# Optimization experiments

Measured on AMD Instinct MI355X. Metric: run time of the kernel, lower is better.

## Reference

```python
import jax, jax.numpy as jnp
import numpy as np

B, N, F, H, F_ = 2048, 8192, 512, 8, 64

def setup_inputs() -> dict:
    key = jax.random.key(0)
    k1, k2, k3, k4 = jax.random.split(key, 4)
    X = jax.random.normal(k1, (B, F), dtype=jnp.float32)
    G = jax.random.normal(k2, (N, F), dtype=jnp.float32)
    W = jax.random.normal(k3, (H, F, F_), dtype=jnp.float32) * 0.05   # per-head kernels
    att = jax.random.normal(k4, (H, 2 * F_), dtype=jnp.float32) * 0.05  # per-head att kernels (2F_,1) flattened
    return {"X": X, "G": G, "W": W, "att": att}

def reference(X, G, W, att):
    f_ = W.shape[-1]
    # Per-head linear transforms
    WhX = jnp.einsum('bf,hfe->hbe', X, W)   # [H,B,F_]
    WhG = jnp.einsum('nf,hfe->hne', G, W)   # [H,N,F_]
    # concat([WhX_i, WhG_j]) @ a  ==  WhX_i @ a1 + WhG_j @ a2  -> avoids tiled [B*N,2F_]
    a1, a2 = att[:, :f_], att[:, f_:]
    e1 = jnp.einsum('hbe,he->hb', WhX, a1)  # [H,B]
    e2 = jnp.einsum('hne,he->hn', WhG, a2)  # [H,N]
    scores = e1[:, :, None] + e2[:, None, :]            # [H,B,N] pairwise logits
    attn = jax.nn.softmax(scores, axis=-1)              # softmax over graph nodes
    out = jnp.einsum('hbn,hne->hbe', attn, WhG)         # weighted aggregate [H,B,F_]
    out = jax.nn.relu(out)                              # concat-mode applies activation per head
    # concat heads -> [B, H*F_]
    return jnp.transpose(out, (1, 0, 2)).reshape(out.shape[1], -1)
```

## Files before the change

### kernel.cpp

```cpp
#include <hip/hip_runtime.h>


#define HF   8
#define FDIM 512
#define FE   64
#define NG   8192
#define BX   2048
#define K2B  256
#define ROWS (NG / K2B)

#define WS_W2 16
#define WS_G  4224
#define WS_S  8384

__global__ __launch_bounds__(256) void k_init(const float* __restrict__ W,
                                              const float* __restrict__ att,
                                              float* __restrict__ ws) {
    int bid = blockIdx.x, tid = threadIdx.x;
    int idx = bid * 256 + tid;
    if (idx < 4096) ws[WS_G + idx] = 0.f;
    if (idx >= 4096 && idx < 4160) ws[WS_S + (idx - 4096)] = 0.f;
    if (idx == 4160) *reinterpret_cast<unsigned int*>(ws) = 0u;

    int o = bid * 64 + (tid >> 2);
    int sub = tid & 3;
    int h = o >> 9;
    const float* wp = W + (size_t)o * FE + sub * 16;
    const float* a2 = att + h * (2 * FE) + FE + sub * 16;
    float s = 0.f;
#pragma unroll
    for (int e = 0; e < 16; e += 4) {
        float4 w4 = *reinterpret_cast<const float4*>(wp + e);
        s += w4.x * a2[e] + w4.y * a2[e + 1] + w4.z * a2[e + 2] + w4.w * a2[e + 3];
    }
    s += __shfl_xor(s, 1, 64);
    s += __shfl_xor(s, 2, 64);
    if (sub == 0) ws[WS_W2 + o] = s;
}

__global__ __launch_bounds__(256, 1) void k_fused(const float* __restrict__ G,
                                                  const float* __restrict__ W,
                                                  float* __restrict__ ws,
                                                  float* __restrict__ out) {
    __shared__ float lds[HF * FDIM];
    __shared__ float s_lds[4 * HF];
    __shared__ float gh[FDIM];
    __shared__ float vp[16][17];
    __shared__ float vrs[16];
    __shared__ float s_h_lds;

    int bid = blockIdx.x, tid = threadIdx.x;
    int wave = tid >> 6, lane = tid & 63;
    const float* w2g = ws + WS_W2;
    float* g = ws + WS_G;
    float* s_slot = ws + WS_S;
    unsigned int* counter = reinterpret_cast<unsigned int*>(ws);

    float4 w2a[HF], w2b[HF];
#pragma unroll
    for (int h = 0; h < HF; ++h) {
        const float* wp = w2g + h * FDIM + lane * 8;
        w2a[h] = *reinterpret_cast<const float4*>(wp);
        w2b[h] = *reinterpret_cast<const float4*>(wp + 4);
    }
    float4 accA[HF], accB[HF];
#pragma unroll
    for (int h = 0; h < HF; ++h) {
        accA[h] = make_float4(0.f, 0.f, 0.f, 0.f);
        accB[h] = make_float4(0.f, 0.f, 0.f, 0.f);
    }
    float s_acc[HF] = {};

    int n0 = bid * ROWS + wave * (ROWS / 4);
    for (int r = 0; r < ROWS / 4; ++r) {
        const float* gp = G + (size_t)(n0 + r) * FDIM + lane * 8;
        float4 g0 = *reinterpret_cast<const float4*>(gp);
        float4 g1 = *reinterpret_cast<const float4*>(gp + 4);
        float e[HF];
#pragma unroll
        for (int h = 0; h < HF; ++h)
            e[h] = g0.x * w2a[h].x + g0.y * w2a[h].y + g0.z * w2a[h].z + g0.w * w2a[h].w
                 + g1.x * w2b[h].x + g1.y * w2b[h].y + g1.z * w2b[h].z + g1.w * w2b[h].w;
#pragma unroll
        for (int off = 32; off > 0; off >>= 1) {
#pragma unroll
            for (int h = 0; h < HF; ++h) e[h] += __shfl_xor(e[h], off, 64);
        }
#pragma unroll
        for (int h = 0; h < HF; ++h) {
            float w = __expf(e[h]);
            s_acc[h] += w;
            accA[h].x = fmaf(w, g0.x, accA[h].x);
            accA[h].y = fmaf(w, g0.y, accA[h].y);
            accA[h].z = fmaf(w, g0.z, accA[h].z);
            accA[h].w = fmaf(w, g0.w, accA[h].w);
            accB[h].x = fmaf(w, g1.x, accB[h].x);
            accB[h].y = fmaf(w, g1.y, accB[h].y);
            accB[h].z = fmaf(w, g1.z, accB[h].z);
            accB[h].w = fmaf(w, g1.w, accB[h].w);
        }
    }

    for (int w = 0; w < 4; ++w) {
        if (wave == w) {
#pragma unroll
            for (int h = 0; h < HF; ++h) {
                float* dst = lds + h * FDIM + lane * 8;
                if (w == 0) {
                    *reinterpret_cast<float4*>(dst)     = accA[h];
                    *reinterpret_cast<float4*>(dst + 4) = accB[h];
                } else {
                    float4 t0 = *reinterpret_cast<float4*>(dst);
                    float4 t1 = *reinterpret_cast<float4*>(dst + 4);
                    t0.x += accA[h].x; t0.y += accA[h].y; t0.z += accA[h].z; t0.w += accA[h].w;
                    t1.x += accB[h].x; t1.y += accB[h].y; t1.z += accB[h].z; t1.w += accB[h].w;
                    *reinterpret_cast<float4*>(dst)     = t0;
                    *reinterpret_cast<float4*>(dst + 4) = t1;
                }
            }
            if (lane == 0) {
#pragma unroll
                for (int h = 0; h < HF; ++h) s_lds[w * HF + h] = s_acc[h];
            }
        }
        __syncthreads();
    }

#pragma unroll
    for (int k = 0; k < 16; ++k) {
        int i = (((k + bid) & 15) << 8) | tid;
        atomicAdd(&g[i], lds[i]);
    }
    if (tid < HF)
        atomicAdd(&s_slot[tid * 8 + (bid & 7)],
                  (s_lds[tid] + s_lds[HF + tid]) + (s_lds[2 * HF + tid] + s_lds[3 * HF + tid]));

    __syncthreads();
    if (tid == 0) {
        __hip_atomic_fetch_add(counter, 1u, __ATOMIC_RELAXED, __HIP_MEMORY_SCOPE_AGENT);
        int iters = 0;
        while (__hip_atomic_load(counter, __ATOMIC_RELAXED, __HIP_MEMORY_SCOPE_AGENT) < K2B) {
            __builtin_amdgcn_s_sleep(2);
            if (++iters > 400000) break;
        }
    }
    __syncthreads();

    int slice = bid & 31, rowchunk = bid >> 5;
    int h = slice >> 2, e0 = (slice & 3) * 16;

    for (int i = tid; i < FDIM; i += 256)
        gh[i] = __hip_atomic_load(&g[h * FDIM + i], __ATOMIC_RELAXED, __HIP_MEMORY_SCOPE_AGENT);
    if (tid == 0) {
        float sv = 0.f;
#pragma unroll
        for (int k = 0; k < 8; ++k)
            sv += __hip_atomic_load(&s_slot[h * 8 + k], __ATOMIC_RELAXED, __HIP_MEMORY_SCOPE_AGENT);
        s_h_lds = sv;
    }
    __syncthreads();

    int j = tid & 15, fg = tid >> 4;
    {
        const float* wp = W + ((size_t)(h * FDIM + fg * 32)) * FE + e0 + j;
        float acc = 0.f;
#pragma unroll 8
        for (int k = 0; k < 32; ++k)
            acc = fmaf(gh[fg * 32 + k], wp[(size_t)k * FE], acc);
        vp[fg][j] = acc;
    }
    __syncthreads();
    if (tid < 16) {
        float v = 0.f;
#pragma unroll
        for (int k = 0; k < 16; ++k) v += vp[k][tid];
        vrs[tid] = fmaxf(v / s_h_lds, 0.f);
    }
    __syncthreads();

    int r = rowchunk * 256 + tid;
    float4* dst = reinterpret_cast<float4*>(out + (size_t)r * FDIM + h * FE + e0);
    float4 o0 = make_float4(vrs[0],  vrs[1],  vrs[2],  vrs[3]);
    float4 o1 = make_float4(vrs[4],  vrs[5],  vrs[6],  vrs[7]);
    float4 o2 = make_float4(vrs[8],  vrs[9],  vrs[10], vrs[11]);
    float4 o3 = make_float4(vrs[12], vrs[13], vrs[14], vrs[15]);
    dst[0] = o0; dst[1] = o1; dst[2] = o2; dst[3] = o3;
}

extern "C" void kernel_launch(void* const* d_in, const int* in_sizes, int n_in,
                              void* d_out, int out_size, void* d_ws, size_t ws_size,
                              hipStream_t stream) {
    const float* G   = (const float*)d_in[1];
    const float* W   = (const float*)d_in[2];
    const float* att = (const float*)d_in[3];
    float* out = (float*)d_out;
    float* ws  = (float*)d_ws;

    k_init <<<64,  256, 0, stream>>>(W, att, ws);
    k_fused<<<K2B, 256, 0, stream>>>(G, W, ws, out);
}
```

Measured before the change: 41.80 us.

## Replace global atomicAdd reduction with per-block partials and 512-thread blocks

The fused kernel now launches 128 blocks of 512 threads instead of 256 blocks of 256 threads. Each block writes its per-head weighted sums and softmax denominators to its own partial slot rather than doing atomicAdd into one shared accumulator. After the grid barrier, each block sums the 128 partials for its head column directly. This removes atomic contention and the zero-init work, but every block now reads 128 partial rows after the barrier and fewer blocks share the streaming of G.

```diff
diff --git a/kernel.cpp b/kernel.cpp
--- a/kernel.cpp
+++ b/kernel.cpp
@@ -6,21 +6,21 @@
 #define FE   64
 #define NG   8192
 #define BX   2048
-#define K2B  256
-#define ROWS (NG / K2B)
-
-#define WS_W2 16
-#define WS_G  4224
-#define WS_S  8384
+#define NBLK 128
+#define NTHR 512
+#define ROWSPB (NG / NBLK)
+
+#define WS_W2   64
+#define WS_SP   4224
+#define WS_PART 8192
 
 __global__ __launch_bounds__(256) void k_init(const float* __restrict__ W,
                                               const float* __restrict__ att,
                                               float* __restrict__ ws) {
     int bid = blockIdx.x, tid = threadIdx.x;
-    int idx = bid * 256 + tid;
-    if (idx < 4096) ws[WS_G + idx] = 0.f;
-    if (idx >= 4096 && idx < 4160) ws[WS_S + (idx - 4096)] = 0.f;
-    if (idx == 4160) *reinterpret_cast<unsigned int*>(ws) = 0u;
+    if (bid == 0 && tid == 0)
+        __hip_atomic_store(reinterpret_cast<unsigned int*>(ws), 0u,
+                           __ATOMIC_RELAXED, __HIP_MEMORY_SCOPE_AGENT);
 
     int o = bid * 64 + (tid >> 2);
     int sub = tid & 3;
@@ -38,22 +38,24 @@
     if (sub == 0) ws[WS_W2 + o] = s;
 }
 
-__global__ __launch_bounds__(256, 1) void k_fused(const float* __restrict__ G,
-                                                  const float* __restrict__ W,
-                                                  float* __restrict__ ws,
-                                                  float* __restrict__ out) {
-    __shared__ float lds[HF * FDIM];
-    __shared__ float s_lds[4 * HF];
+__global__ __launch_bounds__(NTHR, 1) void k_fused(const float* __restrict__ G,
+                                                   const float* __restrict__ W,
+                                                   float* __restrict__ ws,
+                                                   float* __restrict__ out) {
+    __shared__ float lds2[2][HF * FDIM];
+    __shared__ float s_lds[8][HF];
     __shared__ float gh[FDIM];
-    __shared__ float vp[16][17];
+    __shared__ float vp[32][17];
     __shared__ float vrs[16];
+    __shared__ float s_tmp[128];
+    __shared__ float s_red[8];
     __shared__ float s_h_lds;
 
     int bid = blockIdx.x, tid = threadIdx.x;
     int wave = tid >> 6, lane = tid & 63;
     const float* w2g = ws + WS_W2;
-    float* g = ws + WS_G;
-    float* s_slot = ws + WS_S;
+    float* s_part = ws + WS_SP;
+    float* part   = ws + WS_PART;
     unsigned int* counter = reinterpret_cast<unsigned int*>(ws);
 
     float4 w2a[HF], w2b[HF];
@@ -71,8 +73,8 @@
     }
     float s_acc[HF] = {};
 
-    int n0 = bid * ROWS + wave * (ROWS / 4);
-    for (int r = 0; r < ROWS / 4; ++r) {
+    int n0 = bid * ROWSPB + wave * (ROWSPB / 8);
+    for (int r = 0; r < ROWSPB / 8; ++r) {
         const float* gp = G + (size_t)(n0 + r) * FDIM + lane * 8;
         float4 g0 = *reinterpret_cast<const float4*>(gp);
         float4 g1 = *reinterpret_cast<const float4*>(gp + 4);
@@ -101,12 +103,18 @@
         }
     }
 
-    for (int w = 0; w < 4; ++w) {
-        if (wave == w) {
+    if (lane == 0) {
+#pragma unroll
+        for (int h = 0; h < HF; ++h) s_lds[wave][h] = s_acc[h];
+    }
+
+    for (int rnd = 0; rnd < 4; ++rnd) {
+        if ((wave >> 1) == rnd) {
+            int buf = wave & 1;
 #pragma unroll
             for (int h = 0; h < HF; ++h) {
-                float* dst = lds + h * FDIM + lane * 8;
-                if (w == 0) {
+                float* dst = lds2[buf] + h * FDIM + lane * 8;
+                if (rnd == 0) {
                     *reinterpret_cast<float4*>(dst)     = accA[h];
                     *reinterpret_cast<float4*>(dst + 4) = accB[h];
                 } else {
@@ -118,73 +126,92 @@
                     *reinterpret_cast<float4*>(dst + 4) = t1;
                 }
             }
-            if (lane == 0) {
-#pragma unroll
-                for (int h = 0; h < HF; ++h) s_lds[w * HF + h] = s_acc[h];
-            }
         }
         __syncthreads();
     }
 
-#pragma unroll
-    for (int k = 0; k < 16; ++k) {
-        int i = (((k + bid) & 15) << 8) | tid;
-        atomicAdd(&g[i], lds[i]);
-    }
-    if (tid < HF)
-        atomicAdd(&s_slot[tid * 8 + (bid & 7)],
-                  (s_lds[tid] + s_lds[HF + tid]) + (s_lds[2 * HF + tid] + s_lds[3 * HF + tid]));
+    {
+        float* pdst = part + (size_t)bid * (HF * FDIM);
+        for (int i = tid; i < HF * FDIM; i += NTHR)
+            __hip_atomic_store(&pdst[i], lds2[0][i] + lds2[1][i],
+                               __ATOMIC_RELAXED, __HIP_MEMORY_SCOPE_AGENT);
+        if (tid < HF) {
+            float sv = 0.f;
+#pragma unroll
+            for (int w = 0; w < 8; ++w) sv += s_lds[w][tid];
+            __hip_atomic_store(&s_part[bid * HF + tid], sv,
+                               __ATOMIC_RELAXED, __HIP_MEMORY_SCOPE_AGENT);
+        }
+    }
 
     __syncthreads();
     if (tid == 0) {
         __hip_atomic_fetch_add(counter, 1u, __ATOMIC_RELAXED, __HIP_MEMORY_SCOPE_AGENT);
         int iters = 0;
-        while (__hip_atomic_load(counter, __ATOMIC_RELAXED, __HIP_MEMORY_SCOPE_AGENT) < K2B) {
+        while (__hip_atomic_load(counter, __ATOMIC_RELAXED, __HIP_MEMORY_SCOPE_AGENT) < NBLK) {
             __builtin_amdgcn_s_sleep(2);
             if (++iters > 400000) break;
         }
     }
     __syncthreads();
 
-    int slice = bid & 31, rowchunk = bid >> 5;
+    int slice = bid & 31, rc = bid >> 5;
     int h = slice >> 2, e0 = (slice & 3) * 16;
 
-    for (int i = tid; i < FDIM; i += 256)
-        gh[i] = __hip_atomic_load(&g[h * FDIM + i], __ATOMIC_RELAXED, __HIP_MEMORY_SCOPE_AGENT);
+    {
+        float acc = 0.f;
+        const float* pcol = part + (h << 9) + tid;
+#pragma unroll 8
+        for (int p = 0; p < NBLK; ++p)
+            acc += __hip_atomic_load(pcol + (size_t)p * (HF * FDIM),
+                                     __ATOMIC_RELAXED, __HIP_MEMORY_SCOPE_AGENT);
+        gh[tid] = acc;
+    }
+    if (tid < 128)
+        s_tmp[tid] = __hip_atomic_load(&s_part[tid * HF + h],
+                                       __ATOMIC_RELAXED, __HIP_MEMORY_SCOPE_AGENT);
+    __syncthreads();
+    if (tid < 8) {
+        float v = 0.f;
+#pragma unroll
+        for (int k = 0; k < 16; ++k) v += s_tmp[tid * 16 + k];
+        s_red[tid] = v;
+    }
+    __syncthreads();
     if (tid == 0) {
-        float sv = 0.f;
-#pragma unroll
-        for (int k = 0; k < 8; ++k)
-            sv += __hip_atomic_load(&s_slot[h * 8 + k], __ATOMIC_RELAXED, __HIP_MEMORY_SCOPE_AGENT);
-        s_h_lds = sv;
-    }
-    __syncthreads();
-
-    int j = tid & 15, fg = tid >> 4;
-    {
-        const float* wp = W + ((size_t)(h * FDIM + fg * 32)) * FE + e0 + j;
-        float acc = 0.f;
-#pragma unroll 8
-        for (int k = 0; k < 32; ++k)
-            acc = fmaf(gh[fg * 32 + k], wp[(size_t)k * FE], acc);
-        vp[fg][j] = acc;
+        float v = 0.f;
+#pragma unroll
+        for (int k = 0; k < 8; ++k) v += s_red[k];
+        s_h_lds = v;
+    }
+    __syncthreads();
+
+    {
+        int e = tid & 15, fg = tid >> 4;
+        const float* wp = W + (size_t)h * FDIM * FE + (size_t)(fg * 16) * FE + e0 + e;
+        float a = 0.f;
+#pragma unroll
+        for (int k = 0; k < 16; ++k)
+            a = fmaf(gh[fg * 16 + k], wp[(size_t)k * FE], a);
+        vp[fg][e] = a;
     }
     __syncthreads();
     if (tid < 16) {
         float v = 0.f;
 #pragma unroll
-        for (int k = 0; k < 16; ++k) v += vp[k][tid];
+        for (int j = 0; j < 32; ++j) v += vp[j][tid];
         vrs[tid] = fmaxf(v / s_h_lds, 0.f);
     }
     __syncthreads();
 
-    int r = rowchunk * 256 + tid;
-    float4* dst = reinterpret_cast<float4*>(out + (size_t)r * FDIM + h * FE + e0);
-    float4 o0 = make_float4(vrs[0],  vrs[1],  vrs[2],  vrs[3]);
-    float4 o1 = make_float4(vrs[4],  vrs[5],  vrs[6],  vrs[7]);
-    float4 o2 = make_float4(vrs[8],  vrs[9],  vrs[10], vrs[11]);
-    float4 o3 = make_float4(vrs[12], vrs[13], vrs[14], vrs[15]);
-    dst[0] = o0; dst[1] = o1; dst[2] = o2; dst[3] = o3;
+    {
+        int row = rc * 512 + tid;
+        float4* dst = reinterpret_cast<float4*>(out + (size_t)row * FDIM + h * FE + e0);
+        dst[0] = make_float4(vrs[0],  vrs[1],  vrs[2],  vrs[3]);
+        dst[1] = make_float4(vrs[4],  vrs[5],  vrs[6],  vrs[7]);
+        dst[2] = make_float4(vrs[8],  vrs[9],  vrs[10], vrs[11]);
+        dst[3] = make_float4(vrs[12], vrs[13], vrs[14], vrs[15]);
+    }
 }
 
 extern "C" void kernel_launch(void* const* d_in, const int* in_sizes, int n_in,
@@ -196,6 +223,6 @@
     float* out = (float*)d_out;
     float* ws  = (float*)d_ws;
 
-    k_init <<<64,  256, 0, stream>>>(W, att, ws);
-    k_fused<<<K2B, 256, 0, stream>>>(G, W, ws, out);
+    k_init <<<64,   256,  0, stream>>>(W, att, ws);
+    k_fused<<<NBLK, NTHR, 0, stream>>>(G, W, ws, out);
 }
```

Result: slower. 43.53 us (+4.1%).
